# Kernel optimization log

Measured on AMD Instinct MI355X. Metric: run time of the kernel, lower is better.

## Reference

```python
import jax, jax.numpy as jnp
import numpy as np

N, E, IN_DIM, H, D = 50000, 800000, 64, 8, 8
HD = H * D
CLAMP = 5.0


def setup_inputs() -> dict:
    key = jax.random.key(0)
    ks = jax.random.split(key, 13)
    s_in = 1.0 / np.sqrt(IN_DIM)
    s_hd = 1.0 / np.sqrt(HD)
    return {
        "x": jax.random.normal(ks[0], (N, IN_DIM), jnp.float32),
        "edge_attr": jax.random.normal(ks[1], (E, IN_DIM), jnp.float32),
        "edge_index": jax.random.randint(ks[2], (2, E), 0, N, jnp.int32),
        # torch nn.Linear weights are [out_features, in_features]
        "WQ": jax.random.normal(ks[3], (HD, IN_DIM), jnp.float32) * s_in,
        "WK": jax.random.normal(ks[4], (HD, IN_DIM), jnp.float32) * s_in,
        "WV": jax.random.normal(ks[5], (HD, IN_DIM), jnp.float32) * s_in,
        "WEw": jax.random.normal(ks[6], (HD, IN_DIM), jnp.float32) * s_in,
        "WEb": jax.random.normal(ks[7], (HD, IN_DIM), jnp.float32) * s_in,
        "bEb": jax.random.normal(ks[8], (HD,), jnp.float32) * 0.02,
        "WEo": jax.random.normal(ks[9], (HD, HD), jnp.float32) * s_hd,
        "bEo": jax.random.normal(ks[10], (HD,), jnp.float32) * 0.02,
        "Aw": jax.random.normal(ks[11], (D, H, 1), jnp.float32) * s_hd,
        "BW": jax.random.normal(ks[12], (D, H, D), jnp.float32) * s_hd,
    }


def _scatter_softmax(score, dst, num_nodes):
    # score: [E, H, 1]; softmax over edges grouped by dst node
    mx = jax.ops.segment_max(score, dst, num_segments=num_nodes)  # [N,H,1]
    ex = jnp.exp(score - mx[dst])
    den = jax.ops.segment_sum(ex, dst, num_segments=num_nodes)    # [N,H,1]
    return ex / (den[dst] + 1e-16)


def reference(x, edge_attr, edge_index, WQ, WK, WV, WEw, WEb, bEb, WEo, bEo, Aw, BW):
    n = x.shape[0]
    e = edge_attr.shape[0]
    Qh = (x @ WQ.T).reshape(n, H, D)
    Kh = (x @ WK.T).reshape(n, H, D)
    Vh = (x @ WV.T).reshape(n, H, D)
    Ew = (edge_attr @ WEw.T).reshape(e, H, D)
    Eb = (edge_attr @ WEb.T + bEb).reshape(e, H, D)

    dst, src = edge_index[0], edge_index[1]
    conn1 = (Qh[dst] + Kh[src]) * Ew                       # [E,H,D]
    # sqrt(relu(x)) - sqrt(relu(-x)) == sign(x)*sqrt(|x|)
    conn2 = jnp.sign(conn1) * jnp.sqrt(jnp.abs(conn1))
    conn = conn2 + Eb                                      # act = Identity

    Eo_flat = conn.reshape(e, HD) @ WEo.T + bEo            # Oe output [E, H*D]
    Eo = Eo_flat.reshape(e, H, D)

    score = jnp.einsum('ehd,dhc->ehc', conn, Aw)           # [E,H,1]
    score = jnp.clip(score, -CLAMP, CLAMP)
    score = _scatter_softmax(score, dst, n)

    agg = jax.ops.segment_sum(Vh[src] * score, dst, num_segments=n)   # [N,H,D]
    rowV = jax.ops.segment_sum(Eo * score, dst, num_segments=n)       # [N,H,D]
    rowV = jnp.einsum('nhd,dhc->nhc', rowV, BW)
    h_out = agg + rowV                                     # [N,H,D]
    return (h_out, Eo_flat)
```

## Files before the change

kernel.cpp:

```cpp
#include <hip/hip_runtime.h>

#define NN 50000
#define EE 800000
#define NTILES (EE / 128)
#define NB ((NN + 1023) / 1024)

typedef __attribute__((ext_vector_type(8))) short short8;
typedef __attribute__((ext_vector_type(16))) float f32x16;

static __device__ __forceinline__ unsigned short f2bf(float f) {
    unsigned u = __float_as_uint(f);
    u += 0x7fffu + ((u >> 16) & 1u);
    return (unsigned short)(u >> 16);
}
static __device__ __forceinline__ unsigned pack2(float a, float b) {
    return (unsigned)f2bf(a) | ((unsigned)f2bf(b) << 16);
}
static __device__ __forceinline__ float bf2f(unsigned short s) {
    return __uint_as_float((unsigned)s << 16);
}
static __device__ __forceinline__ f32x16 splat16(float v) {
    f32x16 r;
    #pragma unroll
    for (int i = 0; i < 16; ++i) r[i] = v;
    return r;
}

union U8 { short8 v; uint2 u[2]; };

static __device__ __forceinline__ short8 ldsfrag(const unsigned short* rowbase, int k0) {
    U8 t;
    t.u[0] = *(const uint2*)(rowbase + k0);
    t.u[1] = *(const uint2*)(rowbase + k0 + 8);
    return t.v;
}

__global__ __launch_bounds__(256) void qkv_mfma_kernel(
    const float* __restrict__ x,
    const float* __restrict__ WQ, const float* __restrict__ WK, const float* __restrict__ WV,
    float* __restrict__ Qh, float* __restrict__ Kh, float* __restrict__ Vh)
{
    __shared__ unsigned short s_wq[64][68];
    __shared__ unsigned short s_wk[64][68];
    __shared__ unsigned short s_wv[64][68];

    int tid = threadIdx.x;
    #pragma unroll
    for (int t = 0; t < 16; ++t) {
        int idx = t * 256 + tid;
        int r = idx >> 6, c = idx & 63;
        s_wq[r][c] = f2bf(WQ[idx]);
        s_wk[r][c] = f2bf(WK[idx]);
        s_wv[r][c] = f2bf(WV[idx]);
    }
    __syncthreads();

    int wid = tid >> 6, lane = tid & 63;
    int m0 = blockIdx.x * 128 + wid * 32;
    int lo5 = lane & 31, hi = lane >> 5;

    int rowi = m0 + lo5;
    const float* arow = x + (size_t)(rowi < NN ? rowi : NN - 1) * 64;
    short8 af[4];
    #pragma unroll
    for (int ks = 0; ks < 4; ++ks) {
        int k0 = ks * 16 + hi * 4;
        float4 a0 = *(const float4*)(arow + k0);
        float4 a1 = *(const float4*)(arow + k0 + 8);
        U8 t;
        t.u[0] = make_uint2(pack2(a0.x, a0.y), pack2(a0.z, a0.w));
        t.u[1] = make_uint2(pack2(a1.x, a1.y), pack2(a1.z, a1.w));
        af[ks] = t.v;
    }

    #pragma unroll
    for (int nt = 0; nt < 2; ++nt) {
        int n = nt * 32 + lo5;
        f32x16 cQ = splat16(0.f), cK = splat16(0.f), cV = splat16(0.f);
        #pragma unroll
        for (int ks = 0; ks < 4; ++ks) {
            int k0 = ks * 16 + hi * 4;
            cQ = __builtin_amdgcn_mfma_f32_32x32x16_bf16(af[ks], ldsfrag(s_wq[n], k0), cQ, 0, 0, 0);
            cK = __builtin_amdgcn_mfma_f32_32x32x16_bf16(af[ks], ldsfrag(s_wk[n], k0), cK, 0, 0, 0);
            cV = __builtin_amdgcn_mfma_f32_32x32x16_bf16(af[ks], ldsfrag(s_wv[n], k0), cV, 0, 0, 0);
        }
        #pragma unroll
        for (int r = 0; r < 16; ++r) {
            int m = (r & 3) + 8 * (r >> 2) + 4 * hi;
            int gm = m0 + m;
            if (gm < NN) {
                Qh[(size_t)gm * 64 + n] = cQ[r];
                Kh[(size_t)gm * 64 + n] = cK[r];
                Vh[(size_t)gm * 64 + n] = cV[r];
            }
        }
    }
}

__global__ __launch_bounds__(256) void hist_kernel(const int* __restrict__ eidx,
                                                   int* __restrict__ cnt)
{
    int e = blockIdx.x * blockDim.x + threadIdx.x;
    atomicAdd(&cnt[eidx[e]], 1);
}

__global__ __launch_bounds__(1024) void scan1_kernel(const int* __restrict__ cnt,
                                                     int* __restrict__ rowstart,
                                                     int* __restrict__ bsum)
{
    __shared__ int buf[1024];
    int tid = threadIdx.x;
    int i = blockIdx.x * 1024 + tid;
    int v = (i < NN) ? cnt[i] : 0;
    buf[tid] = v;
    __syncthreads();
    for (int off = 1; off < 1024; off <<= 1) {
        int t = (tid >= off) ? buf[tid - off] : 0;
        __syncthreads();
        buf[tid] += t;
        __syncthreads();
    }
    if (i < NN) rowstart[i] = buf[tid] - v;
    if (tid == 1023) bsum[blockIdx.x] = buf[1023];
}

__global__ __launch_bounds__(64) void scan2_kernel(const int* __restrict__ bsum,
                                                   int* __restrict__ boff,
                                                   int* __restrict__ rowstart)
{
    int lane = threadIdx.x;
    int v = (lane < NB) ? bsum[lane] : 0;
    int s = v;
    #pragma unroll
    for (int off = 1; off < 64; off <<= 1) {
        int t = __shfl_up(s, off, 64);
        if (lane >= off) s += t;
    }
    if (lane < NB) boff[lane] = s - v;
    if (lane == 63) rowstart[NN] = s;
}

__global__ __launch_bounds__(1024) void scan3_kernel(int* __restrict__ rowstart,
                                                     const int* __restrict__ boff,
                                                     int* __restrict__ cursor)
{
    int i = blockIdx.x * 1024 + threadIdx.x;
    if (i < NN) {
        int r = rowstart[i] + boff[blockIdx.x];
        rowstart[i] = r;
        cursor[i] = r;
    }
}

__global__ __launch_bounds__(256) void scatter_kernel(const int* __restrict__ eidx,
                                                      int* __restrict__ cursor,
                                                      int* __restrict__ perm,
                                                      int* __restrict__ psrc,
                                                      int* __restrict__ inv)
{
    int e = blockIdx.x * blockDim.x + threadIdx.x;
    int dst = eidx[e];
    int pos = atomicAdd(&cursor[dst], 1);
    perm[pos] = e;
    psrc[pos] = eidx[EE + e];
    inv[e] = pos;
}

__global__ __launch_bounds__(256) void edge_mfma_kernel(
    const float* __restrict__ eattr, const int* __restrict__ eidx,
    const int* __restrict__ inv,
    const float* __restrict__ WEw, const float* __restrict__ WEb, const float* __restrict__ bEb,
    const float* __restrict__ WEo, const float* __restrict__ bEo, const float* __restrict__ Aw,
    const float* __restrict__ Qh, const float* __restrict__ Kh,
    float* __restrict__ Eo_out, float* __restrict__ exbuf)
{
    __shared__ unsigned short s_wew[64][68];
    __shared__ unsigned short s_web[64][68];
    __shared__ unsigned short s_weo[64][68];
    __shared__ unsigned short s_cq[4][32][68];

    int tid = threadIdx.x;
    #pragma unroll
    for (int t = 0; t < 16; ++t) {
        int idx = t * 256 + tid;
        int r = idx >> 6, c = idx & 63;
        s_wew[r][c] = f2bf(WEw[idx]);
        s_web[r][c] = f2bf(WEb[idx]);
        s_weo[r][c] = f2bf(WEo[idx]);
    }
    __syncthreads();

    int wid = tid >> 6, lane = tid & 63;
    int lo5 = lane & 31, hi = lane >> 5;
    int mm = lane >> 4;
    int cc = (lane & 15) * 4;

    float awv[32];
    #pragma unroll
    for (int ks = 0; ks < 4; ++ks)
        #pragma unroll
        for (int i = 0; i < 8; ++i) {
            int k = ks * 16 + hi * 4 + (i & 3) + ((i >> 2) << 3);
            awv[ks * 8 + i] = Aw[(k & 7) * 8 + (k >> 3)];
        }
    float bEbn0 = bEb[lo5], bEbn1 = bEb[32 + lo5];
    float bEon0 = bEo[lo5], bEon1 = bEo[32 + lo5];

    for (int tile = blockIdx.x; tile < NTILES; tile += gridDim.x) {
        int e0 = tile * 128 + wid * 32;
        int pos = inv[e0 + lo5];

        #pragma unroll
        for (int t = 0; t < 8; ++t) {
            int m = t * 4 + mm;
            int e = e0 + m;
            int dst = eidx[e], src = eidx[EE + e];
            float4 q = *(const float4*)(Qh + (size_t)dst * 64 + cc);
            float4 k = *(const float4*)(Kh + (size_t)src * 64 + cc);
            *(uint2*)&s_cq[wid][m][cc] = make_uint2(pack2(q.x + k.x, q.y + k.y),
                                                    pack2(q.z + k.z, q.w + k.w));
        }

        short8 af[4];
        {
            const float* arow = eattr + (size_t)(e0 + lo5) * 64;
            #pragma unroll
            for (int ks = 0; ks < 4; ++ks) {
                int k0 = ks * 16 + hi * 4;
                float4 a0 = *(const float4*)(arow + k0);
                float4 a1 = *(const float4*)(arow + k0 + 8);
                U8 t;
                t.u[0] = make_uint2(pack2(a0.x, a0.y), pack2(a0.z, a0.w));
                t.u[1] = make_uint2(pack2(a1.x, a1.y), pack2(a1.z, a1.w));
                af[ks] = t.v;
            }
        }

        #pragma unroll
        for (int nt = 0; nt < 2; ++nt) {
            int n = nt * 32 + lo5;
            f32x16 cEw = splat16(0.f), cEb = splat16(0.f);
            #pragma unroll
            for (int ks = 0; ks < 4; ++ks) {
                int k0 = ks * 16 + hi * 4;
                cEw = __builtin_amdgcn_mfma_f32_32x32x16_bf16(af[ks], ldsfrag(s_wew[n], k0), cEw, 0, 0, 0);
                cEb = __builtin_amdgcn_mfma_f32_32x32x16_bf16(af[ks], ldsfrag(s_web[n], k0), cEb, 0, 0, 0);
            }
            float bEbn = nt ? bEbn1 : bEbn0;
            #pragma unroll
            for (int r = 0; r < 16; ++r) {
                int m = (r & 3) + 8 * (r >> 2) + 4 * hi;
                float qk = bf2f(s_cq[wid][m][n]);
                float c1 = qk * cEw[r];
                float c2 = copysignf(sqrtf(fabsf(c1)), c1);
                s_cq[wid][m][n] = f2bf(c2 + cEb[r] + bEbn);
            }
        }

        short8 ca[4];
        #pragma unroll
        for (int ks = 0; ks < 4; ++ks) {
            int k0 = ks * 16 + hi * 4;
            ca[ks] = ldsfrag(s_cq[wid][lo5], k0);
        }

        {
            float sc[8];
            #pragma unroll
            for (int h2 = 0; h2 < 8; ++h2) sc[h2] = 0.f;
            #pragma unroll
            for (int ks = 0; ks < 4; ++ks)
                #pragma unroll
                for (int i = 0; i < 8; ++i) {
                    float cv = bf2f((unsigned short)ca[ks][i]);
                    sc[2 * ks + (i >> 2)] = fmaf(cv, awv[ks * 8 + i], sc[2 * ks + (i >> 2)]);
                }
            #pragma unroll
            for (int h2 = 0; h2 < 8; ++h2) {
                sc[h2] += __shfl_xor(sc[h2], 32, 64);
                sc[h2] = fminf(fmaxf(sc[h2], -5.0f), 5.0f);
                sc[h2] = __expf(sc[h2]);
            }
            if (hi == 0) {
                *(float4*)(exbuf + (size_t)pos * 8 + 0) = make_float4(sc[0], sc[1], sc[2], sc[3]);
                *(float4*)(exbuf + (size_t)pos * 8 + 4) = make_float4(sc[4], sc[5], sc[6], sc[7]);
            }
        }

        #pragma unroll
        for (int nt = 0; nt < 2; ++nt) {
            int n = nt * 32 + lo5;
            f32x16 cO = splat16(nt ? bEon1 : bEon0);
            #pragma unroll
            for (int ks = 0; ks < 4; ++ks) {
                int k0 = ks * 16 + hi * 4;
                cO = __builtin_amdgcn_mfma_f32_32x32x16_bf16(ca[ks], ldsfrag(s_weo[n], k0), cO, 0, 0, 0);
            }
            #pragma unroll
            for (int r = 0; r < 16; ++r) {
                int m = (r & 3) + 8 * (r >> 2) + 4 * hi;
                Eo_out[(size_t)(e0 + m) * 64 + n] = cO[r];
            }
        }
    }
}

__global__ __launch_bounds__(256) void node_kernel(
    const int* __restrict__ rowstart, const int* __restrict__ perm,
    const int* __restrict__ psrc,
    const float* __restrict__ exbuf, const float* __restrict__ Eo,
    const float* __restrict__ Vh, const float* __restrict__ BW,
    float* __restrict__ hout)
{
    int n = (blockIdx.x * blockDim.x + threadIdx.x) >> 6;
    int lane = threadIdx.x & 63;
    int h = lane >> 3, d = lane & 7;

    int beg = rowstart[n], end = rowstart[n + 1];
    float agg0 = 0.f, rv0 = 0.f, den0 = 0.f;
    float agg1 = 0.f, rv1 = 0.f, den1 = 0.f;
    int j = beg;
    for (; j + 1 < end; j += 2) {
        int ea = perm[j],     sa = psrc[j];
        int eb = perm[j + 1], sb = psrc[j + 1];
        float xa = exbuf[(size_t)j * 8 + h];
        float xb = exbuf[(size_t)(j + 1) * 8 + h];
        agg0 = fmaf(xa, Vh[(size_t)sa * 64 + lane], agg0);
        rv0  = fmaf(xa, Eo[(size_t)ea * 64 + lane], rv0);
        den0 += xa;
        agg1 = fmaf(xb, Vh[(size_t)sb * 64 + lane], agg1);
        rv1  = fmaf(xb, Eo[(size_t)eb * 64 + lane], rv1);
        den1 += xb;
    }
    if (j < end) {
        int ea = perm[j], sa = psrc[j];
        float xa = exbuf[(size_t)j * 8 + h];
        agg0 = fmaf(xa, Vh[(size_t)sa * 64 + lane], agg0);
        rv0  = fmaf(xa, Eo[(size_t)ea * 64 + lane], rv0);
        den0 += xa;
    }
    float agg = agg0 + agg1, rv = rv0 + rv1, den = den0 + den1;
    float inv = (den > 0.f) ? (1.0f / den) : 0.f;

    float acc = agg;
    #pragma unroll
    for (int dd = 0; dd < 8; ++dd) {
        float rvd = __shfl(rv, (h << 3) + dd, 64);
        acc = fmaf(rvd, BW[dd * 64 + (h << 3) + d], acc);
    }
    hout[(size_t)n * 64 + lane] = acc * inv;
}

extern "C" void kernel_launch(void* const* d_in, const int* in_sizes, int n_in,
                              void* d_out, int out_size, void* d_ws, size_t ws_size,
                              hipStream_t stream)
{
    const float* x    = (const float*)d_in[0];
    const float* ea   = (const float*)d_in[1];
    const int*   eidx = (const int*)  d_in[2];
    const float* WQ   = (const float*)d_in[3];
    const float* WK   = (const float*)d_in[4];
    const float* WV   = (const float*)d_in[5];
    const float* WEw  = (const float*)d_in[6];
    const float* WEb  = (const float*)d_in[7];
    const float* bEb  = (const float*)d_in[8];
    const float* WEo  = (const float*)d_in[9];
    const float* bEo  = (const float*)d_in[10];
    const float* Aw   = (const float*)d_in[11];
    const float* BW   = (const float*)d_in[12];

    float* hout   = (float*)d_out;
    float* Eo_out = hout + (size_t)NN * 64;

    float* Qh    = (float*)d_ws;
    float* Kh    = Qh + (size_t)NN * 64;
    float* Vh    = Kh + (size_t)NN * 64;
    float* exbuf = Vh + (size_t)NN * 64;
    int* cnt      = (int*)(exbuf + (size_t)EE * 8);
    int* rowstart = cnt + NN;
    int* perm     = rowstart + (NN + 1);
    int* psrc     = perm + EE;
    int* invp     = psrc + EE;
    int* bsum     = invp + EE;
    int* boff     = bsum + 64;

    hipMemsetAsync(cnt, 0, (size_t)NN * sizeof(int), stream);

    hist_kernel<<<EE / 256, 256, 0, stream>>>(eidx, cnt);
    scan1_kernel<<<NB, 1024, 0, stream>>>(cnt, rowstart, bsum);
    scan2_kernel<<<1, 64, 0, stream>>>(bsum, boff, rowstart);
    scan3_kernel<<<NB, 1024, 0, stream>>>(rowstart, boff, cnt);
    scatter_kernel<<<EE / 256, 256, 0, stream>>>(eidx, cnt, perm, psrc, invp);

    qkv_mfma_kernel<<<(NN + 127) / 128, 256, 0, stream>>>(x, WQ, WK, WV, Qh, Kh, Vh);

    edge_mfma_kernel<<<2080, 256, 0, stream>>>(ea, eidx, invp, WEw, WEb, bEb, WEo, bEo, Aw,
                                               Qh, Kh, Eo_out, exbuf);

    node_kernel<<<(NN * 64) / 256, 256, 0, stream>>>(rowstart, perm, psrc,
                                                     exbuf, Eo_out, Vh, BW, hout);
}
```

Baseline: 364.9 us.

## Gather Q+K directly into registers, pack CSR edges, enlarge edge blocks

The edge kernel now gathers Qh[dst]+Kh[src] straight into MFMA accumulator-layout registers in fp32, instead of staging a bf16 sum through shared memory. Each lane does scalar per-column gathers instead of float4 row loads. The CSR perm and src arrays are interleaved into one int2 array so the node kernel needs a single load per edge. The edge kernel also moves to 512-thread blocks with 256 edges per tile and a 512-block grid, and LDS row padding shrinks from 68 to 66. The cost is less coalesced gathers, and the padding change may alter bank-conflict behaviour.

```diff
diff --git a/kernel.cpp b/kernel.cpp
--- a/kernel.cpp
+++ b/kernel.cpp
@@ -2,7 +2,8 @@
 
 #define NN 50000
 #define EE 800000
-#define NTILES (EE / 128)
+#define EPT 256
+#define NT8 (EE / EPT)
 #define NB ((NN + 1023) / 1024)
 
 typedef __attribute__((ext_vector_type(8))) short short8;
@@ -40,9 +41,9 @@
     const float* __restrict__ WQ, const float* __restrict__ WK, const float* __restrict__ WV,
     float* __restrict__ Qh, float* __restrict__ Kh, float* __restrict__ Vh)
 {
-    __shared__ unsigned short s_wq[64][68];
-    __shared__ unsigned short s_wk[64][68];
-    __shared__ unsigned short s_wv[64][68];
+    __shared__ unsigned short s_wq[64][66];
+    __shared__ unsigned short s_wk[64][66];
+    __shared__ unsigned short s_wv[64][66];
 
     int tid = threadIdx.x;
     #pragma unroll
@@ -154,19 +155,17 @@
 
 __global__ __launch_bounds__(256) void scatter_kernel(const int* __restrict__ eidx,
                                                       int* __restrict__ cursor,
-                                                      int* __restrict__ perm,
-                                                      int* __restrict__ psrc,
+                                                      int2* __restrict__ edges_csr,
                                                       int* __restrict__ inv)
 {
     int e = blockIdx.x * blockDim.x + threadIdx.x;
     int dst = eidx[e];
     int pos = atomicAdd(&cursor[dst], 1);
-    perm[pos] = e;
-    psrc[pos] = eidx[EE + e];
+    edges_csr[pos] = make_int2(e, eidx[EE + e]);
     inv[e] = pos;
 }
 
-__global__ __launch_bounds__(256) void edge_mfma_kernel(
+__global__ __launch_bounds__(512) void edge_mfma_kernel(
     const float* __restrict__ eattr, const int* __restrict__ eidx,
     const int* __restrict__ inv,
     const float* __restrict__ WEw, const float* __restrict__ WEb, const float* __restrict__ bEb,
@@ -174,15 +173,15 @@
     const float* __restrict__ Qh, const float* __restrict__ Kh,
     float* __restrict__ Eo_out, float* __restrict__ exbuf)
 {
-    __shared__ unsigned short s_wew[64][68];
-    __shared__ unsigned short s_web[64][68];
-    __shared__ unsigned short s_weo[64][68];
-    __shared__ unsigned short s_cq[4][32][68];
+    __shared__ unsigned short s_wew[64][66];
+    __shared__ unsigned short s_web[64][66];
+    __shared__ unsigned short s_weo[64][66];
+    __shared__ unsigned short s_conn[8][32][66];
 
     int tid = threadIdx.x;
     #pragma unroll
-    for (int t = 0; t < 16; ++t) {
-        int idx = t * 256 + tid;
+    for (int t = 0; t < 8; ++t) {
+        int idx = t * 512 + tid;
         int r = idx >> 6, c = idx & 63;
         s_wew[r][c] = f2bf(WEw[idx]);
         s_web[r][c] = f2bf(WEb[idx]);
@@ -192,8 +191,6 @@
 
     int wid = tid >> 6, lane = tid & 63;
     int lo5 = lane & 31, hi = lane >> 5;
-    int mm = lane >> 4;
-    int cc = (lane & 15) * 4;
 
     float awv[32];
     #pragma unroll
@@ -206,20 +203,9 @@
     float bEbn0 = bEb[lo5], bEbn1 = bEb[32 + lo5];
     float bEon0 = bEo[lo5], bEon1 = bEo[32 + lo5];
 
-    for (int tile = blockIdx.x; tile < NTILES; tile += gridDim.x) {
-        int e0 = tile * 128 + wid * 32;
+    for (int tile = blockIdx.x; tile < NT8; tile += gridDim.x) {
+        int e0 = tile * EPT + wid * 32;
         int pos = inv[e0 + lo5];
-
-        #pragma unroll
-        for (int t = 0; t < 8; ++t) {
-            int m = t * 4 + mm;
-            int e = e0 + m;
-            int dst = eidx[e], src = eidx[EE + e];
-            float4 q = *(const float4*)(Qh + (size_t)dst * 64 + cc);
-            float4 k = *(const float4*)(Kh + (size_t)src * 64 + cc);
-            *(uint2*)&s_cq[wid][m][cc] = make_uint2(pack2(q.x + k.x, q.y + k.y),
-                                                    pack2(q.z + k.z, q.w + k.w));
-        }
 
         short8 af[4];
         {
@@ -239,6 +225,18 @@
         #pragma unroll
         for (int nt = 0; nt < 2; ++nt) {
             int n = nt * 32 + lo5;
+
+            float qk[16];
+            #pragma unroll
+            for (int rr = 0; rr < 4; ++rr) {
+                int4 d4 = *(const int4*)(eidx + e0 + rr * 8 + hi * 4);
+                int4 s4 = *(const int4*)(eidx + EE + e0 + rr * 8 + hi * 4);
+                qk[rr * 4 + 0] = Qh[(size_t)d4.x * 64 + n] + Kh[(size_t)s4.x * 64 + n];
+                qk[rr * 4 + 1] = Qh[(size_t)d4.y * 64 + n] + Kh[(size_t)s4.y * 64 + n];
+                qk[rr * 4 + 2] = Qh[(size_t)d4.z * 64 + n] + Kh[(size_t)s4.z * 64 + n];
+                qk[rr * 4 + 3] = Qh[(size_t)d4.w * 64 + n] + Kh[(size_t)s4.w * 64 + n];
+            }
+
             f32x16 cEw = splat16(0.f), cEb = splat16(0.f);
             #pragma unroll
             for (int ks = 0; ks < 4; ++ks) {
@@ -250,10 +248,9 @@
             #pragma unroll
             for (int r = 0; r < 16; ++r) {
                 int m = (r & 3) + 8 * (r >> 2) + 4 * hi;
-                float qk = bf2f(s_cq[wid][m][n]);
-                float c1 = qk * cEw[r];
+                float c1 = qk[r] * cEw[r];
                 float c2 = copysignf(sqrtf(fabsf(c1)), c1);
-                s_cq[wid][m][n] = f2bf(c2 + cEb[r] + bEbn);
+                s_conn[wid][m][n] = f2bf(c2 + cEb[r] + bEbn);
             }
         }
 
@@ -261,7 +258,7 @@
         #pragma unroll
         for (int ks = 0; ks < 4; ++ks) {
             int k0 = ks * 16 + hi * 4;
-            ca[ks] = ldsfrag(s_cq[wid][lo5], k0);
+            ca[ks] = ldsfrag(s_conn[wid][lo5], k0);
         }
 
         {
@@ -306,8 +303,7 @@
 }
 
 __global__ __launch_bounds__(256) void node_kernel(
-    const int* __restrict__ rowstart, const int* __restrict__ perm,
-    const int* __restrict__ psrc,
+    const int* __restrict__ rowstart, const int2* __restrict__ edges_csr,
     const float* __restrict__ exbuf, const float* __restrict__ Eo,
     const float* __restrict__ Vh, const float* __restrict__ BW,
     float* __restrict__ hout)
@@ -321,22 +317,22 @@
     float agg1 = 0.f, rv1 = 0.f, den1 = 0.f;
     int j = beg;
     for (; j + 1 < end; j += 2) {
-        int ea = perm[j],     sa = psrc[j];
-        int eb = perm[j + 1], sb = psrc[j + 1];
+        int2 ea = edges_csr[j];
+        int2 eb = edges_csr[j + 1];
         float xa = exbuf[(size_t)j * 8 + h];
         float xb = exbuf[(size_t)(j + 1) * 8 + h];
-        agg0 = fmaf(xa, Vh[(size_t)sa * 64 + lane], agg0);
-        rv0  = fmaf(xa, Eo[(size_t)ea * 64 + lane], rv0);
+        agg0 = fmaf(xa, Vh[(size_t)ea.y * 64 + lane], agg0);
+        rv0  = fmaf(xa, Eo[(size_t)ea.x * 64 + lane], rv0);
         den0 += xa;
-        agg1 = fmaf(xb, Vh[(size_t)sb * 64 + lane], agg1);
-        rv1  = fmaf(xb, Eo[(size_t)eb * 64 + lane], rv1);
+        agg1 = fmaf(xb, Vh[(size_t)eb.y * 64 + lane], agg1);
+        rv1  = fmaf(xb, Eo[(size_t)eb.x * 64 + lane], rv1);
         den1 += xb;
     }
     if (j < end) {
-        int ea = perm[j], sa = psrc[j];
+        int2 ea = edges_csr[j];
         float xa = exbuf[(size_t)j * 8 + h];
-        agg0 = fmaf(xa, Vh[(size_t)sa * 64 + lane], agg0);
-        rv0  = fmaf(xa, Eo[(size_t)ea * 64 + lane], rv0);
+        agg0 = fmaf(xa, Vh[(size_t)ea.y * 64 + lane], agg0);
+        rv0  = fmaf(xa, Eo[(size_t)ea.x * 64 + lane], rv0);
         den0 += xa;
     }
     float agg = agg0 + agg1, rv = rv0 + rv1, den = den0 + den1;
@@ -378,9 +374,8 @@
     float* exbuf = Vh + (size_t)NN * 64;
     int* cnt      = (int*)(exbuf + (size_t)EE * 8);
     int* rowstart = cnt + NN;
-    int* perm     = rowstart + (NN + 1);
-    int* psrc     = perm + EE;
-    int* invp     = psrc + EE;
+    int2* edges_csr = (int2*)(rowstart + NN + 2);
+    int* invp     = (int*)(edges_csr + EE);
     int* bsum     = invp + EE;
     int* boff     = bsum + 64;
 
@@ -390,13 +385,13 @@
     scan1_kernel<<<NB, 1024, 0, stream>>>(cnt, rowstart, bsum);
     scan2_kernel<<<1, 64, 0, stream>>>(bsum, boff, rowstart);
     scan3_kernel<<<NB, 1024, 0, stream>>>(rowstart, boff, cnt);
-    scatter_kernel<<<EE / 256, 256, 0, stream>>>(eidx, cnt, perm, psrc, invp);
+    scatter_kernel<<<EE / 256, 256, 0, stream>>>(eidx, cnt, edges_csr, invp);
 
     qkv_mfma_kernel<<<(NN + 127) / 128, 256, 0, stream>>>(x, WQ, WK, WV, Qh, Kh, Vh);
 
-    edge_mfma_kernel<<<2080, 256, 0, stream>>>(ea, eidx, invp, WEw, WEb, bEb, WEo, bEo, Aw,
-                                               Qh, Kh, Eo_out, exbuf);
-
-    node_kernel<<<(NN * 64) / 256, 256, 0, stream>>>(rowstart, perm, psrc,
+    edge_mfma_kernel<<<512, 512, 0, stream>>>(ea, eidx, invp, WEw, WEb, bEb, WEo, bEo, Aw,
+                                              Qh, Kh, Eo_out, exbuf);
+
+    node_kernel<<<(NN * 64) / 256, 256, 0, stream>>>(rowstart, edges_csr,
                                                      exbuf, Eo_out, Vh, BW, hout);
 }
```

Result: slower. 386.2 us (+5.8%).

## Use hardware bf16 pack, interleave CSR arrays, prefetch edge attrs, unroll node gather

Applied to the files above, without the earlier changes.

Replaces the software round-to-nearest bf16 packing with the v_cvt_pk_bf16_f32 instruction and vectorizes the weight staging loads into float2. Merges the perm and psrc arrays into one int2 CSR array so each edge needs a single load. Hoists the edge_attr loads ahead of the Q/K gather so they can be in flight together, and unrolls the node aggregation loop by four for more outstanding gathers. These aim to cut ALU work and memory latency, at the cost of higher register pressure.

```diff
diff --git a/kernel.cpp b/kernel.cpp
--- a/kernel.cpp
+++ b/kernel.cpp
@@ -13,8 +13,10 @@
     u += 0x7fffu + ((u >> 16) & 1u);
     return (unsigned short)(u >> 16);
 }
-static __device__ __forceinline__ unsigned pack2(float a, float b) {
-    return (unsigned)f2bf(a) | ((unsigned)f2bf(b) << 16);
+static __device__ __forceinline__ unsigned cvt_pk(float lo, float hi) {
+    unsigned r;
+    asm("v_cvt_pk_bf16_f32 %0, %1, %2" : "=v"(r) : "v"(lo), "v"(hi));
+    return r;
 }
 static __device__ __forceinline__ float bf2f(unsigned short s) {
     return __uint_as_float((unsigned)s << 16);
@@ -46,12 +48,15 @@
 
     int tid = threadIdx.x;
     #pragma unroll
-    for (int t = 0; t < 16; ++t) {
-        int idx = t * 256 + tid;
+    for (int t = 0; t < 8; ++t) {
+        int idx = (t * 256 + tid) * 2;
         int r = idx >> 6, c = idx & 63;
-        s_wq[r][c] = f2bf(WQ[idx]);
-        s_wk[r][c] = f2bf(WK[idx]);
-        s_wv[r][c] = f2bf(WV[idx]);
+        float2 w = *(const float2*)(WQ + idx);
+        *(unsigned*)&s_wq[r][c] = cvt_pk(w.x, w.y);
+        w = *(const float2*)(WK + idx);
+        *(unsigned*)&s_wk[r][c] = cvt_pk(w.x, w.y);
+        w = *(const float2*)(WV + idx);
+        *(unsigned*)&s_wv[r][c] = cvt_pk(w.x, w.y);
     }
     __syncthreads();
 
@@ -68,8 +73,8 @@
         float4 a0 = *(const float4*)(arow + k0);
         float4 a1 = *(const float4*)(arow + k0 + 8);
         U8 t;
-        t.u[0] = make_uint2(pack2(a0.x, a0.y), pack2(a0.z, a0.w));
-        t.u[1] = make_uint2(pack2(a1.x, a1.y), pack2(a1.z, a1.w));
+        t.u[0] = make_uint2(cvt_pk(a0.x, a0.y), cvt_pk(a0.z, a0.w));
+        t.u[1] = make_uint2(cvt_pk(a1.x, a1.y), cvt_pk(a1.z, a1.w));
         af[ks] = t.v;
     }
 
@@ -154,15 +159,13 @@
 
 __global__ __launch_bounds__(256) void scatter_kernel(const int* __restrict__ eidx,
                                                       int* __restrict__ cursor,
-                                                      int* __restrict__ perm,
-                                                      int* __restrict__ psrc,
+                                                      int2* __restrict__ edges_csr,
                                                       int* __restrict__ inv)
 {
     int e = blockIdx.x * blockDim.x + threadIdx.x;
     int dst = eidx[e];
     int pos = atomicAdd(&cursor[dst], 1);
-    perm[pos] = e;
-    psrc[pos] = eidx[EE + e];
+    edges_csr[pos] = make_int2(e, eidx[EE + e]);
     inv[e] = pos;
 }
 
@@ -181,12 +184,15 @@
 
     int tid = threadIdx.x;
     #pragma unroll
-    for (int t = 0; t < 16; ++t) {
-        int idx = t * 256 + tid;
+    for (int t = 0; t < 8; ++t) {
+        int idx = (t * 256 + tid) * 2;
         int r = idx >> 6, c = idx & 63;
-        s_wew[r][c] = f2bf(WEw[idx]);
-        s_web[r][c] = f2bf(WEb[idx]);
-        s_weo[r][c] = f2bf(WEo[idx]);
+        float2 w = *(const float2*)(WEw + idx);
+        *(unsigned*)&s_wew[r][c] = cvt_pk(w.x, w.y);
+        w = *(const float2*)(WEb + idx);
+        *(unsigned*)&s_web[r][c] = cvt_pk(w.x, w.y);
+        w = *(const float2*)(WEo + idx);
+        *(unsigned*)&s_weo[r][c] = cvt_pk(w.x, w.y);
     }
     __syncthreads();
 
@@ -209,6 +215,17 @@
     for (int tile = blockIdx.x; tile < NTILES; tile += gridDim.x) {
         int e0 = tile * 128 + wid * 32;
         int pos = inv[e0 + lo5];
+
+        float4 ea[8];
+        {
+            const float* arow = eattr + (size_t)(e0 + lo5) * 64;
+            #pragma unroll
+            for (int ks = 0; ks < 4; ++ks) {
+                int k0 = ks * 16 + hi * 4;
+                ea[2 * ks + 0] = *(const float4*)(arow + k0);
+                ea[2 * ks + 1] = *(const float4*)(arow + k0 + 8);
+            }
+        }
 
         #pragma unroll
         for (int t = 0; t < 8; ++t) {
@@ -217,23 +234,18 @@
             int dst = eidx[e], src = eidx[EE + e];
             float4 q = *(const float4*)(Qh + (size_t)dst * 64 + cc);
             float4 k = *(const float4*)(Kh + (size_t)src * 64 + cc);
-            *(uint2*)&s_cq[wid][m][cc] = make_uint2(pack2(q.x + k.x, q.y + k.y),
-                                                    pack2(q.z + k.z, q.w + k.w));
+            *(uint2*)&s_cq[wid][m][cc] = make_uint2(cvt_pk(q.x + k.x, q.y + k.y),
+                                                    cvt_pk(q.z + k.z, q.w + k.w));
         }
 
         short8 af[4];
-        {
-            const float* arow = eattr + (size_t)(e0 + lo5) * 64;
-            #pragma unroll
-            for (int ks = 0; ks < 4; ++ks) {
-                int k0 = ks * 16 + hi * 4;
-                float4 a0 = *(const float4*)(arow + k0);
-                float4 a1 = *(const float4*)(arow + k0 + 8);
-                U8 t;
-                t.u[0] = make_uint2(pack2(a0.x, a0.y), pack2(a0.z, a0.w));
-                t.u[1] = make_uint2(pack2(a1.x, a1.y), pack2(a1.z, a1.w));
-                af[ks] = t.v;
-            }
+        #pragma unroll
+        for (int ks = 0; ks < 4; ++ks) {
+            float4 a0 = ea[2 * ks + 0], a1 = ea[2 * ks + 1];
+            U8 t;
+            t.u[0] = make_uint2(cvt_pk(a0.x, a0.y), cvt_pk(a0.z, a0.w));
+            t.u[1] = make_uint2(cvt_pk(a1.x, a1.y), cvt_pk(a1.z, a1.w));
+            af[ks] = t.v;
         }
 
         #pragma unroll
@@ -306,8 +318,7 @@
 }
 
 __global__ __launch_bounds__(256) void node_kernel(
-    const int* __restrict__ rowstart, const int* __restrict__ perm,
-    const int* __restrict__ psrc,
+    const int* __restrict__ rowstart, const int2* __restrict__ edges_csr,
     const float* __restrict__ exbuf, const float* __restrict__ Eo,
     const float* __restrict__ Vh, const float* __restrict__ BW,
     float* __restrict__ hout)
@@ -320,24 +331,34 @@
     float agg0 = 0.f, rv0 = 0.f, den0 = 0.f;
     float agg1 = 0.f, rv1 = 0.f, den1 = 0.f;
     int j = beg;
-    for (; j + 1 < end; j += 2) {
-        int ea = perm[j],     sa = psrc[j];
-        int eb = perm[j + 1], sb = psrc[j + 1];
-        float xa = exbuf[(size_t)j * 8 + h];
-        float xb = exbuf[(size_t)(j + 1) * 8 + h];
-        agg0 = fmaf(xa, Vh[(size_t)sa * 64 + lane], agg0);
-        rv0  = fmaf(xa, Eo[(size_t)ea * 64 + lane], rv0);
-        den0 += xa;
-        agg1 = fmaf(xb, Vh[(size_t)sb * 64 + lane], agg1);
-        rv1  = fmaf(xb, Eo[(size_t)eb * 64 + lane], rv1);
-        den1 += xb;
-    }
-    if (j < end) {
-        int ea = perm[j], sa = psrc[j];
-        float xa = exbuf[(size_t)j * 8 + h];
-        agg0 = fmaf(xa, Vh[(size_t)sa * 64 + lane], agg0);
-        rv0  = fmaf(xa, Eo[(size_t)ea * 64 + lane], rv0);
-        den0 += xa;
+    for (; j + 3 < end; j += 4) {
+        int2 p0 = edges_csr[j + 0];
+        int2 p1 = edges_csr[j + 1];
+        int2 p2 = edges_csr[j + 2];
+        int2 p3 = edges_csr[j + 3];
+        float x0 = exbuf[(size_t)(j + 0) * 8 + h];
+        float x1 = exbuf[(size_t)(j + 1) * 8 + h];
+        float x2 = exbuf[(size_t)(j + 2) * 8 + h];
+        float x3 = exbuf[(size_t)(j + 3) * 8 + h];
+        float v0 = Vh[(size_t)p0.y * 64 + lane];
+        float o0 = Eo[(size_t)p0.x * 64 + lane];
+        float v1 = Vh[(size_t)p1.y * 64 + lane];
+        float o1 = Eo[(size_t)p1.x * 64 + lane];
+        float v2 = Vh[(size_t)p2.y * 64 + lane];
+        float o2 = Eo[(size_t)p2.x * 64 + lane];
+        float v3 = Vh[(size_t)p3.y * 64 + lane];
+        float o3 = Eo[(size_t)p3.x * 64 + lane];
+        agg0 = fmaf(x0, v0, agg0); rv0 = fmaf(x0, o0, rv0); den0 += x0;
+        agg1 = fmaf(x1, v1, agg1); rv1 = fmaf(x1, o1, rv1); den1 += x1;
+        agg0 = fmaf(x2, v2, agg0); rv0 = fmaf(x2, o2, rv0); den0 += x2;
+        agg1 = fmaf(x3, v3, agg1); rv1 = fmaf(x3, o3, rv1); den1 += x3;
+    }
+    for (; j < end; ++j) {
+        int2 p0 = edges_csr[j];
+        float x0 = exbuf[(size_t)j * 8 + h];
+        agg0 = fmaf(x0, Vh[(size_t)p0.y * 64 + lane], agg0);
+        rv0  = fmaf(x0, Eo[(size_t)p0.x * 64 + lane], rv0);
+        den0 += x0;
     }
     float agg = agg0 + agg1, rv = rv0 + rv1, den = den0 + den1;
     float inv = (den > 0.f) ? (1.0f / den) : 0.f;
@@ -378,9 +399,8 @@
     float* exbuf = Vh + (size_t)NN * 64;
     int* cnt      = (int*)(exbuf + (size_t)EE * 8);
     int* rowstart = cnt + NN;
-    int* perm     = rowstart + (NN + 1);
-    int* psrc     = perm + EE;
-    int* invp     = psrc + EE;
+    int2* edges_csr = (int2*)(rowstart + NN + 2);
+    int* invp     = (int*)(edges_csr + EE);
     int* bsum     = invp + EE;
     int* boff     = bsum + 64;
 
@@ -390,13 +410,13 @@
     scan1_kernel<<<NB, 1024, 0, stream>>>(cnt, rowstart, bsum);
     scan2_kernel<<<1, 64, 0, stream>>>(bsum, boff, rowstart);
     scan3_kernel<<<NB, 1024, 0, stream>>>(rowstart, boff, cnt);
-    scatter_kernel<<<EE / 256, 256, 0, stream>>>(eidx, cnt, perm, psrc, invp);
+    scatter_kernel<<<EE / 256, 256, 0, stream>>>(eidx, cnt, edges_csr, invp);
 
     qkv_mfma_kernel<<<(NN + 127) / 128, 256, 0, stream>>>(x, WQ, WK, WV, Qh, Kh, Vh);
 
-    edge_mfma_kernel<<<2080, 256, 0, stream>>>(ea, eidx, invp, WEw, WEb, bEb, WEo, bEo, Aw,
-                                               Qh, Kh, Eo_out, exbuf);
-
-    node_kernel<<<(NN * 64) / 256, 256, 0, stream>>>(rowstart, perm, psrc,
+    edge_mfma_kernel<<<2080, 256, 0, stream>>>(ea, eidx, invp, WEw, WEb, bEb,
+                                               WEo, bEo, Aw, Qh, Kh, Eo_out, exbuf);
+
+    node_kernel<<<(NN * 64) / 256, 256, 0, stream>>>(rowstart, edges_csr,
                                                      exbuf, Eo_out, Vh, BW, hout);
 }
```

Measured after the change: 368.4 us (median of 5 runs). Within noise of the previous version (+1.0%).
